# Performance work log

Hardware: AMD Instinct MI355X
Metric: run time of the kernel (lower is better)

## Reference

```python
import jax, jax.numpy as jnp
import numpy as np

B, S, H = 2, 2048, 2048
NH, NKV = 16, 4
HD = H // NH           # 128
THETA = 1000000.0


def setup_inputs() -> dict:
    key = jax.random.key(0)
    ks = jax.random.split(key, 6)
    s = 0.02
    hidden_states = jax.random.normal(ks[0], (B, S, H), jnp.float32)
    # additive causal mask, broadcast over batch and heads
    causal = jnp.tril(jnp.ones((S, S), bool))
    attention_mask = jnp.where(causal, 0.0, -1e9).astype(jnp.float32)[None, None]
    position_ids = jnp.broadcast_to(jnp.arange(S, dtype=jnp.int32), (B, S))
    wq = jax.random.normal(ks[1], (H, H), jnp.float32) * s
    bq = jnp.zeros((H,), jnp.float32)
    wk = jax.random.normal(ks[2], (H, NKV * HD), jnp.float32) * s
    bk = jnp.zeros((NKV * HD,), jnp.float32)
    wv = jax.random.normal(ks[3], (H, NKV * HD), jnp.float32) * s
    bv = jnp.zeros((NKV * HD,), jnp.float32)
    wo = jax.random.normal(ks[4], (H, H), jnp.float32) * s
    return {"hidden_states": hidden_states, "attention_mask": attention_mask,
            "position_ids": position_ids, "wq": wq, "bq": bq, "wk": wk, "bk": bk,
            "wv": wv, "bv": bv, "wo": wo}


def _rope(x, cos, sin):
    # x: [B,S,h,HD]; interleaved-pair rotation == complex multiply in original
    x2 = x.reshape(*x.shape[:-1], HD // 2, 2)
    x0, x1 = x2[..., 0], x2[..., 1]
    r0 = x0 * cos - x1 * sin
    r1 = x0 * sin + x1 * cos
    return jnp.stack([r0, r1], axis=-1).reshape(x.shape).astype(jnp.float32)


def reference(hidden_states, attention_mask, position_ids, wq, bq, wk, bk, wv, bv, wo):
    bf = jnp.bfloat16
    x = hidden_states.astype(bf)
    # projections in bf16, as flax Dense(dtype=bfloat16)
    q = (x @ wq.astype(bf) + bq.astype(bf)).reshape(B, S, NH, HD)
    k = (x @ wk.astype(bf) + bk.astype(bf)).reshape(B, S, NKV, HD)
    v = (x @ wv.astype(bf) + bv.astype(bf)).reshape(B, S, NKV, HD)
    # RoPE: freqs_cis = exp(1j * pos * inv_freq); real rotation form, identical math
    pos = position_ids[0].astype(jnp.float32)                       # [S]
    inv = 1.0 / (THETA ** (jnp.arange(0, HD, 2, dtype=jnp.float32) / HD))  # [HD/2]
    ang = pos[:, None] * inv[None, :]                               # [S, HD/2]
    cos = jnp.cos(ang)[None, :, None, :]
    sin = jnp.sin(ang)[None, :, None, :]
    q = _rope(q, cos, sin)   # cast to float32 per module dtype
    k = _rope(k, cos, sin)
    cache_k, cache_v = k, v.astype(jnp.float32)
    rep = NH // NKV
    kr = jnp.repeat(k, rep, axis=2)                                 # [B,S,NH,HD]
    vr = jnp.repeat(v, rep, axis=2).astype(jnp.float32)
    scale = 1.0 / np.sqrt(HD).astype(np.float32)
    scores = jnp.einsum('bqhd,bkhd->bhqk', q, kr) * scale + attention_mask
    # float64 cast in original is a no-op w/o x64; softmax runs in float32
    probs = jnp.clip(jax.nn.softmax(scores, axis=-1), 1e-9, 1.0 - 1e-9)
    attn = jnp.einsum('bhqk,bkhd->bqhd', probs, vr).reshape(B, S, H)
    out = attn.astype(bf) @ wo.astype(bf)   # o_proj, no bias, bf16
    return out, (cache_k, cache_v)
```

## Files before the change

### kernel.cpp

```cpp
#include <hip/hip_runtime.h>
#include <hip/hip_bf16.h>
#include <math.h>

#define B_    2
#define S_    2048
#define H_    2048
#define NH_   16
#define NKV_  4
#define HD_   128
#define M_    (B_*S_)
#define NKVH_ (NKV_*HD_)
#define QKVN  3072
#define PSTR  72

typedef __bf16 bf16x8 __attribute__((ext_vector_type(8)));
typedef __bf16 bf16x4 __attribute__((ext_vector_type(4)));
typedef float  f32x4  __attribute__((ext_vector_type(4)));

__device__ __forceinline__ float bf2f(unsigned short u){
  unsigned int i = ((unsigned int)u) << 16; float f;
  __builtin_memcpy(&f, &i, 4); return f;
}
__device__ __forceinline__ unsigned short f2bf(float f){
  unsigned int i; __builtin_memcpy(&i, &f, 4);
  unsigned int r = (i + 0x7fffu + ((i >> 16) & 1u)) >> 16;
  return (unsigned short)r;
}
__device__ __forceinline__ float fast_exp2(float x){
  float r; asm("v_exp_f32 %0, %1" : "=v"(r) : "v"(x)); return r;
}

#define GLOAD_LDS16(g, l) __builtin_amdgcn_global_load_lds( \
    (const __attribute__((address_space(1))) void*)(g), \
    (__attribute__((address_space(3))) void*)(l), 16, 0, 0)

__global__ void k_f32_to_bf16(const float* __restrict__ in, unsigned short* __restrict__ out, int n4){
  int idx = blockIdx.x * blockDim.x + threadIdx.x;
  if (idx >= n4) return;
  float4 v = reinterpret_cast<const float4*>(in)[idx];
  ushort4 o; o.x = f2bf(v.x); o.y = f2bf(v.y); o.z = f2bf(v.z); o.w = f2bf(v.w);
  reinterpret_cast<ushort4*>(out)[idx] = o;
}

__device__ __forceinline__ void tr_tile(const float* __restrict__ W, unsigned short* __restrict__ Wt,
                                        int N, int kx, int ny, int t,
                                        unsigned short (*tile)[36]){
  int k0 = kx * 32, n0 = ny * 32;
  int kr = t >> 3, nc = (t & 7) * 4;
  float4 v = *reinterpret_cast<const float4*>(&W[(size_t)(k0 + kr) * N + n0 + nc]);
  tile[kr][nc+0] = f2bf(v.x); tile[kr][nc+1] = f2bf(v.y);
  tile[kr][nc+2] = f2bf(v.z); tile[kr][nc+3] = f2bf(v.w);
  __syncthreads();
  int nr = t >> 3, kc = (t & 7) * 4;
  ushort4 o;
  o.x = tile[kc+0][nr]; o.y = tile[kc+1][nr]; o.z = tile[kc+2][nr]; o.w = tile[kc+3][nr];
  *reinterpret_cast<ushort4*>(&Wt[(size_t)(n0 + nr) * H_ + k0 + kc]) = o;
}

__global__ __launch_bounds__(256) void k_prep(
    const float* __restrict__ wq, const float* __restrict__ wk,
    const float* __restrict__ wv, const float* __restrict__ wo,
    const int* __restrict__ pos,
    const float* __restrict__ bq, const float* __restrict__ bk, const float* __restrict__ bv,
    unsigned short* __restrict__ WqT, unsigned short* __restrict__ WkT,
    unsigned short* __restrict__ WvT, unsigned short* __restrict__ WoT,
    float2* __restrict__ tab, float* __restrict__ biasQKV)
{
  __shared__ unsigned short tile[32][36];
  const int bidx = blockIdx.x, t = threadIdx.x;
  if (bidx < 4096) {
    tr_tile(wq, WqT, H_, bidx & 63, bidx >> 6, t, tile);
  } else if (bidx < 5120) {
    int i = bidx - 4096; tr_tile(wk, WkT, NKVH_, i & 63, i >> 6, t, tile);
  } else if (bidx < 6144) {
    int i = bidx - 5120; tr_tile(wv, WvT, NKVH_, i & 63, i >> 6, t, tile);
  } else if (bidx < 10240) {
    int i = bidx - 6144; tr_tile(wo, WoT, H_, i & 63, i >> 6, t, tile);
  } else if (bidx < 10752) {
    int idx = (bidx - 10240) * 256 + t;
    int s = idx >> 6, i = idx & 63;
    float p = (float)pos[s];
    float inv = expf(-(float)i * (13.815510557964274f / 64.0f));
    float ang = p * inv;
    tab[idx] = make_float2(cosf(ang), sinf(ang));
  } else {
    int i = (bidx - 10752) * 256 + t;
    if (i < QKVN)
      biasQKV[i] = (i < H_) ? bq[i] : (i < H_ + NKVH_ ? bk[i - H_] : bv[i - H_ - NKVH_]);
  }
}

__global__ __launch_bounds__(256) void k_postqkv(
    unsigned short* __restrict__ QKV, const float2* __restrict__ tab,
    float* __restrict__ cacheK,
    unsigned short* __restrict__ Vt, float* __restrict__ cacheV)
{
  __shared__ unsigned short tile[32][36];
  const int bidx = blockIdx.x, t = threadIdx.x;
  if (bidx < 2048) {
    int idx = bidx * 256 + t;
    int row = idx >> 7;
    int col0 = (idx & 127) * 4;
    int s = row & (S_ - 1);
    int i0 = (col0 & (HD_ - 1)) >> 1;
    unsigned short* p = QKV + (size_t)row * QKVN + H_ + col0;
    ushort4 v = *reinterpret_cast<ushort4*>(p);
    float2 t0 = tab[(s << 6) + i0], t1 = tab[(s << 6) + i0 + 1];
    float x0 = bf2f(v.x), x1 = bf2f(v.y), x2 = bf2f(v.z), x3 = bf2f(v.w);
    float r0 = x0 * t0.x - x1 * t0.y;
    float r1 = x0 * t0.y + x1 * t0.x;
    float r2 = x2 * t1.x - x3 * t1.y;
    float r3 = x2 * t1.y + x3 * t1.x;
    ushort4 o; o.x = f2bf(r0); o.y = f2bf(r1); o.z = f2bf(r2); o.w = f2bf(r3);
    *reinterpret_cast<ushort4*>(p) = o;
    float4 c; c.x = r0; c.y = r1; c.z = r2; c.w = r3;
    reinterpret_cast<float4*>(cacheK)[idx] = c;
  } else {
    int i = bidx - 2048;
    int s0 = (i & 63) * 32, c0 = ((i >> 6) & 15) * 32, b = i >> 10;
    int sr = t >> 3, cc = (t & 7) * 4;
    ushort4 v = *reinterpret_cast<const ushort4*>(
        &QKV[(size_t)(b * S_ + s0 + sr) * QKVN + H_ + NKVH_ + c0 + cc]);
    tile[sr][cc+0] = v.x; tile[sr][cc+1] = v.y; tile[sr][cc+2] = v.z; tile[sr][cc+3] = v.w;
    float4 cf; cf.x = bf2f(v.x); cf.y = bf2f(v.y); cf.z = bf2f(v.z); cf.w = bf2f(v.w);
    *reinterpret_cast<float4*>(&cacheV[(size_t)(b * S_ + s0 + sr) * NKVH_ + c0 + cc]) = cf;
    __syncthreads();
    int cr = t >> 3, sc = (t & 7) * 4;
    ushort4 o;
    o.x = tile[sc+0][cr]; o.y = tile[sc+1][cr]; o.z = tile[sc+2][cr]; o.w = tile[sc+3][cr];
    *reinterpret_cast<ushort4*>(&Vt[(size_t)(b * NKVH_ + c0 + cr) * S_ + s0 + sc]) = o;
  }
}

__global__ __launch_bounds__(256, 2) void k_gemm128(
    const unsigned short* __restrict__ A,
    const unsigned short* __restrict__ Bt,
    const float* __restrict__ bias,
    unsigned short* __restrict__ Cb,
    float* __restrict__ Cf,
    int M, int N, int K)
{
  __shared__ unsigned short As[2][128 * 64];
  __shared__ unsigned short Bs[2][128 * 64];
  const int nbn = N >> 7;
  const int nwg = gridDim.x;
  int bid = blockIdx.x;
  if ((nwg & 7) == 0) bid = (bid & 7) * (nwg >> 3) + (bid >> 3);
  const int bm = bid / nbn, bn = bid % nbn;
  const int tid = threadIdx.x, lane = tid & 63, wave = tid >> 6;
  const int wr = wave >> 1, wc = wave & 1;
  const int gm0 = bm << 7, gn0 = bn << 7;
  const int l15 = lane & 15, lhi = lane >> 4;
  const int srow8 = lane >> 3;
  const int sch   = (lane & 7) ^ srow8;

  f32x4 acc[4][4];
  f32x4 zero = {0.f, 0.f, 0.f, 0.f};
  #pragma unroll
  for (int m = 0; m < 4; m++)
    #pragma unroll
    for (int n = 0; n < 4; n++) acc[m][n] = zero;

  const int nt = K >> 6;

  auto STAGE_P = [&](int kt, int bi, int p){
    int seg = p * 4 + wave;
    int row = seg * 8 + srow8;
    GLOAD_LDS16(A  + (size_t)(gm0 + row) * K + kt * 64 + sch * 8,
                &As[bi][seg * 512]);
    GLOAD_LDS16(Bt + (size_t)(gn0 + row) * K + kt * 64 + sch * 8,
                &Bs[bi][seg * 512]);
  };

  #pragma unroll
  for (int p = 0; p < 4; p++) STAGE_P(0, 0, p);
  __syncthreads();

  for (int kt = 0; kt < nt; ++kt) {
    const int cur = kt & 1, nxt = cur ^ 1;
    const bool pre = (kt + 1 < nt);

    bf16x8 bfr[4][2];
    #pragma unroll
    for (int nf = 0; nf < 4; nf++) {
      int row = wc * 64 + nf * 16 + l15;
      #pragma unroll
      for (int kk = 0; kk < 2; kk++)
        bfr[nf][kk] = *reinterpret_cast<const bf16x8*>(
            &Bs[cur][row * 64 + (((kk << 2) + lhi) ^ (row & 7)) * 8]);
    }

    #pragma unroll
    for (int mf = 0; mf < 4; mf++) {
      if (pre) STAGE_P(kt + 1, nxt, mf);
      bf16x8 af[2];
      int row = wr * 64 + mf * 16 + l15;
      #pragma unroll
      for (int kk = 0; kk < 2; kk++)
        af[kk] = *reinterpret_cast<const bf16x8*>(
            &As[cur][row * 64 + (((kk << 2) + lhi) ^ (row & 7)) * 8]);
      __builtin_amdgcn_s_setprio(1);
      #pragma unroll
      for (int nf = 0; nf < 4; nf++)
        #pragma unroll
        for (int kk = 0; kk < 2; kk++)
          acc[mf][nf] = __builtin_amdgcn_mfma_f32_16x16x32_bf16(
              af[kk], bfr[nf][kk], acc[mf][nf], 0, 0, 0);
      __builtin_amdgcn_s_setprio(0);
    }
    __syncthreads();
  }

  #pragma unroll
  for (int mf = 0; mf < 4; mf++) {
    #pragma unroll
    for (int nf = 0; nf < 4; nf++) {
      int col = gn0 + wc * 64 + nf * 16 + l15;
      float bv = bias ? bias[col] : 0.0f;
      #pragma unroll
      for (int r = 0; r < 4; r++) {
        int row = gm0 + wr * 64 + mf * 16 + lhi * 4 + r;
        size_t idx = (size_t)row * N + col;
        float v = acc[mf][nf][r] + bv;
        if (Cf) Cf[idx] = bf2f(f2bf(v));
        else    Cb[idx] = f2bf(v);
      }
    }
  }
}

__device__ __forceinline__ bf16x8 rope8(ushort4 a, ushort4 b, const float2* __restrict__ tb, float mul){
  unsigned short u[8];
  float2 c;
  c = tb[0]; { float x0=bf2f(a.x), x1=bf2f(a.y); u[0]=f2bf((x0*c.x-x1*c.y)*mul); u[1]=f2bf((x0*c.y+x1*c.x)*mul); }
  c = tb[1]; { float x0=bf2f(a.z), x1=bf2f(a.w); u[2]=f2bf((x0*c.x-x1*c.y)*mul); u[3]=f2bf((x0*c.y+x1*c.x)*mul); }
  c = tb[2]; { float x0=bf2f(b.x), x1=bf2f(b.y); u[4]=f2bf((x0*c.x-x1*c.y)*mul); u[5]=f2bf((x0*c.y+x1*c.x)*mul); }
  c = tb[3]; { float x0=bf2f(b.z), x1=bf2f(b.w); u[6]=f2bf((x0*c.x-x1*c.y)*mul); u[7]=f2bf((x0*c.y+x1*c.x)*mul); }
  bf16x8 r; __builtin_memcpy(&r, u, 16); return r;
}

__global__ __launch_bounds__(256, 2) void k_attn(
    const unsigned short* __restrict__ QKV,
    const unsigned short* __restrict__ Vt,
    const float2* __restrict__ tab,
    unsigned short* __restrict__ O)
{
  __shared__ unsigned short Ks[2][64 * 128];
  __shared__ unsigned short Vs[128 * 64];
  __shared__ unsigned short Plds[4][32 * PSTR];
  const int qb = blockIdx.x;
  const int h = blockIdx.y, b = blockIdx.z;
  const int tid = threadIdx.x, lane = tid & 63, wave = tid >> 6;
  const int l15 = lane & 15, lhi = lane >> 4;
  const int q0a = qb * 64 + wave * 16;
  const int q0b = (31 - qb) * 64 + wave * 16;
  const int kvh = h >> 2;
  const float scale = 0.08838834764831845f;
  const float LOG2E = 1.4426950408889634f;
  const float SHIFT2 = 23.083120654223414f;

  const unsigned short* Kg = QKV + (size_t)(b * S_) * QKVN + H_ + kvh * HD_;
  const unsigned short* Vg = Vt + (size_t)(b * NKV_ + kvh) * HD_ * S_;

  bf16x8 qfa[4], qfb[4];
  {
    const unsigned short* qa = QKV + (size_t)(b * S_ + q0a + l15) * QKVN + h * HD_ + lhi * 8;
    const unsigned short* qbp = QKV + (size_t)(b * S_ + q0b + l15) * QKVN + h * HD_ + lhi * 8;
    const float2* ta = tab + (size_t)(q0a + l15) * 64;
    const float2* tb = tab + (size_t)(q0b + l15) * 64;
    #pragma unroll
    for (int t = 0; t < 4; t++) {
      int i0 = t * 16 + lhi * 4;
      ushort4 a0 = *reinterpret_cast<const ushort4*>(qa + t * 32);
      ushort4 a1 = *reinterpret_cast<const ushort4*>(qa + t * 32 + 4);
      ushort4 b0 = *reinterpret_cast<const ushort4*>(qbp + t * 32);
      ushort4 b1 = *reinterpret_cast<const ushort4*>(qbp + t * 32 + 4);
      qfa[t] = rope8(a0, a1, ta + i0, scale);
      qfb[t] = rope8(b0, b1, tb + i0, scale);
    }
  }

  f32x4 oa[8], ob[8];
  f32x4 zero = {0.f, 0.f, 0.f, 0.f};
  #pragma unroll
  for (int d = 0; d < 8; d++) { oa[d] = zero; ob[d] = zero; }
  float la = 0.f, lb = 0.f;

  unsigned short* pl = &Plds[wave][0];
  const int ktmax = 31 - qb;
  const int krow = tid >> 4, kch = tid & 15;
  const int vrow = tid >> 3, vch = tid & 7;

  auto STAGE_K = [&](int kt, int bi){
    #pragma unroll
    for (int p = 0; p < 4; p++) {
      int r = p * 16 + krow;
      int cs = kch ^ (r & 7);
      GLOAD_LDS16(Kg + (size_t)(kt * 64 + r) * QKVN + cs * 8, &Ks[bi][(p * 16 + 4 * wave) * 128]);
    }
  };
  auto STAGE_V = [&](int kt){
    #pragma unroll
    for (int p = 0; p < 4; p++) {
      int r = p * 32 + vrow;
      int cs = vch ^ (r & 7);
      GLOAD_LDS16(Vg + (size_t)r * S_ + kt * 64 + cs * 8, &Vs[(p * 32 + 8 * wave) * 64]);
    }
  };

  STAGE_K(0, 0);
  __syncthreads();
  int cur = 0;

  for (int kt = 0; kt <= ktmax; ++kt) {
    STAGE_V(kt);
    if (kt < ktmax) STAGE_K(kt + 1, cur ^ 1);
    const bool doA = (kt <= qb);

    f32x4 sca[4], scb[4];
    #pragma unroll
    for (int c = 0; c < 4; c++) { sca[c] = zero; scb[c] = zero; }
    __builtin_amdgcn_s_setprio(1);
    #pragma unroll
    for (int c = 0; c < 4; c++) {
      int rk = c * 16 + l15;
      #pragma unroll
      for (int t = 0; t < 4; t++) {
        bf16x8 kf = *reinterpret_cast<const bf16x8*>(
            &Ks[cur][rk * 128 + (((t << 2) + lhi) ^ (rk & 7)) * 8]);
        scb[c] = __builtin_amdgcn_mfma_f32_16x16x32_bf16(kf, qfb[t], scb[c], 0, 0, 0);
        if (doA) sca[c] = __builtin_amdgcn_mfma_f32_16x16x32_bf16(kf, qfa[t], sca[c], 0, 0, 0);
      }
    }
    __builtin_amdgcn_s_setprio(0);

    {
      int qiB = q0b + l15;
      float acc = 0.f;
      #pragma unroll
      for (int c = 0; c < 4; c++) {
        float pv[4];
        #pragma unroll
        for (int r = 0; r < 4; r++) {
          int key = kt * 64 + c * 16 + lhi * 4 + r;
          float sv = (key > qiB) ? -1e30f : scb[c][r];
          pv[r] = fast_exp2(fmaf(sv, LOG2E, -SHIFT2));
          acc += pv[r];
        }
        bf16x4 w;
        w[0] = (__bf16)pv[0]; w[1] = (__bf16)pv[1]; w[2] = (__bf16)pv[2]; w[3] = (__bf16)pv[3];
        *reinterpret_cast<bf16x4*>(&pl[(16 + l15) * PSTR + c * 16 + lhi * 4]) = w;
      }
      lb += acc;
    }
    if (doA) {
      int qiA = q0a + l15;
      float acc = 0.f;
      #pragma unroll
      for (int c = 0; c < 4; c++) {
        float pv[4];
        #pragma unroll
        for (int r = 0; r < 4; r++) {
          int key = kt * 64 + c * 16 + lhi * 4 + r;
          float sv = (key > qiA) ? -1e30f : sca[c][r];
          pv[r] = fast_exp2(fmaf(sv, LOG2E, -SHIFT2));
          acc += pv[r];
        }
        bf16x4 w;
        w[0] = (__bf16)pv[0]; w[1] = (__bf16)pv[1]; w[2] = (__bf16)pv[2]; w[3] = (__bf16)pv[3];
        *reinterpret_cast<bf16x4*>(&pl[l15 * PSTR + c * 16 + lhi * 4]) = w;
      }
      la += acc;
    }
    asm volatile("" ::: "memory");
    bf16x8 pfb0 = *reinterpret_cast<const bf16x8*>(&pl[(16 + l15) * PSTR + lhi * 8]);
    bf16x8 pfb1 = *reinterpret_cast<const bf16x8*>(&pl[(16 + l15) * PSTR + 32 + lhi * 8]);
    bf16x8 pfa0 = pfb0, pfa1 = pfb1;
    if (doA) {
      pfa0 = *reinterpret_cast<const bf16x8*>(&pl[l15 * PSTR + lhi * 8]);
      pfa1 = *reinterpret_cast<const bf16x8*>(&pl[l15 * PSTR + 32 + lhi * 8]);
    }
    asm volatile("" ::: "memory");

    __syncthreads();

    __builtin_amdgcn_s_setprio(1);
    #pragma unroll
    for (int d = 0; d < 8; d++) {
      int rv = d * 16 + l15;
      bf16x8 vf0 = *reinterpret_cast<const bf16x8*>(&Vs[rv * 64 + (lhi ^ (rv & 7)) * 8]);
      bf16x8 vf1 = *reinterpret_cast<const bf16x8*>(&Vs[rv * 64 + ((4 + lhi) ^ (rv & 7)) * 8]);
      ob[d] = __builtin_amdgcn_mfma_f32_16x16x32_bf16(pfb0, vf0, ob[d], 0, 0, 0);
      ob[d] = __builtin_amdgcn_mfma_f32_16x16x32_bf16(pfb1, vf1, ob[d], 0, 0, 0);
      if (doA) {
        oa[d] = __builtin_amdgcn_mfma_f32_16x16x32_bf16(pfa0, vf0, oa[d], 0, 0, 0);
        oa[d] = __builtin_amdgcn_mfma_f32_16x16x32_bf16(pfa1, vf1, oa[d], 0, 0, 0);
      }
    }
    __builtin_amdgcn_s_setprio(0);

    __syncthreads();
    cur ^= 1;
  }

  la += __shfl_xor(la, 16); la += __shfl_xor(la, 32);
  lb += __shfl_xor(lb, 16); lb += __shfl_xor(lb, 32);

  #pragma unroll
  for (int r = 0; r < 4; r++) {
    int src = (lane & 48) | (lhi * 4 + r);
    float invA = 1.0f / __shfl(la, src);
    float invB = 1.0f / __shfl(lb, src);
    size_t offA = (size_t)(b * S_ + q0a + lhi * 4 + r) * H_ + h * HD_;
    size_t offB = (size_t)(b * S_ + q0b + lhi * 4 + r) * H_ + h * HD_;
    #pragma unroll
    for (int d = 0; d < 8; d++) {
      O[offA + d * 16 + l15] = f2bf(oa[d][r] * invA);
      O[offB + d * 16 + l15] = f2bf(ob[d][r] * invB);
    }
  }
}

extern "C" void kernel_launch(void* const* d_in, const int* in_sizes, int n_in,
                              void* d_out, int out_size, void* d_ws, size_t ws_size,
                              hipStream_t stream) {
  const float* hidden = (const float*)d_in[0];
  const int*   pos    = (const int*)d_in[2];
  const float* wq     = (const float*)d_in[3];
  const float* bq     = (const float*)d_in[4];
  const float* wk     = (const float*)d_in[5];
  const float* bk     = (const float*)d_in[6];
  const float* wv     = (const float*)d_in[7];
  const float* bv     = (const float*)d_in[8];
  const float* wo     = (const float*)d_in[9];

  float* outF   = (float*)d_out;
  float* cacheK = outF + (size_t)M_ * H_;
  float* cacheV = cacheK + (size_t)M_ * NKVH_;

  char* w = (char*)d_ws;
  unsigned short* Xbf  = (unsigned short*)w; w += (size_t)M_ * H_ * 2;
  unsigned short* WqT  = (unsigned short*)w; w += (size_t)H_ * H_ * 2;
  unsigned short* WkT  = (unsigned short*)w; w += (size_t)NKVH_ * H_ * 2;
  unsigned short* WvT  = (unsigned short*)w; w += (size_t)NKVH_ * H_ * 2;
  unsigned short* WoT  = (unsigned short*)w; w += (size_t)H_ * H_ * 2;
  unsigned short* QKVw = (unsigned short*)w; w += (size_t)M_ * QKVN * 2;
  unsigned short* Vt   = (unsigned short*)w; w += (size_t)M_ * NKVH_ * 2;
  float2*         tab  = (float2*)w;         w += (size_t)S_ * 64 * sizeof(float2);
  float*       biasQKV = (float*)w;          w += QKVN * sizeof(float);
  unsigned short* Ao   = Xbf;

  k_f32_to_bf16<<<(M_ * H_ / 4) / 256, 256, 0, stream>>>(hidden, Xbf, M_ * H_ / 4);
  k_prep<<<10764, 256, 0, stream>>>(wq, wk, wv, wo, pos, bq, bk, bv,
                                    WqT, WkT, WvT, WoT, tab, biasQKV);
  k_gemm128<<<(M_ >> 7) * (QKVN >> 7), 256, 0, stream>>>(Xbf, WqT, biasQKV, QKVw, nullptr, M_, QKVN, H_);
  k_postqkv<<<4096, 256, 0, stream>>>(QKVw, tab, cacheK, Vt, cacheV);
  k_attn<<<dim3(16, NH_, B_), 256, 0, stream>>>(QKVw, Vt, tab, Ao);
  k_gemm128<<<(M_ >> 7) * (H_ >> 7), 256, 0, stream>>>(Ao, WoT, nullptr, nullptr, outF, M_, H_, H_);
}
```

Measured before the change: 214.9 us.

## Replace double-buffered swizzled GEMM with single-buffer K=32 tile loop

The projection GEMM drops its double-buffered 64-wide K tiles with XOR-swizzled LDS layout and interleaved prefetch in favour of a simple single-buffered loop over 32-wide K slices, synced twice per step. LDS per block shrinks and launch bounds rise to 3 blocks per CU, aiming for more occupancy to hide latency. In exchange, global loads no longer overlap with MFMA work, there are twice as many barriers, and the unswizzled layout may cause LDS bank conflicts.

```diff
diff --git a/kernel.cpp b/kernel.cpp
--- a/kernel.cpp
+++ b/kernel.cpp
@@ -132,7 +132,7 @@
   }
 }
 
-__global__ __launch_bounds__(256, 2) void k_gemm128(
+__global__ __launch_bounds__(256, 3) void k_gemm_bt(
     const unsigned short* __restrict__ A,
     const unsigned short* __restrict__ Bt,
     const float* __restrict__ bias,
@@ -140,8 +140,8 @@
     float* __restrict__ Cf,
     int M, int N, int K)
 {
-  __shared__ unsigned short As[2][128 * 64];
-  __shared__ unsigned short Bs[2][128 * 64];
+  __shared__ unsigned short As[128 * 32];
+  __shared__ unsigned short Bs[128 * 32];
   const int nbn = N >> 7;
   const int nwg = gridDim.x;
   int bid = blockIdx.x;
@@ -151,8 +151,7 @@
   const int wr = wave >> 1, wc = wave & 1;
   const int gm0 = bm << 7, gn0 = bn << 7;
   const int l15 = lane & 15, lhi = lane >> 4;
-  const int srow8 = lane >> 3;
-  const int sch   = (lane & 7) ^ srow8;
+  const int srow = lane >> 2, scol = (lane & 3) * 8;
 
   f32x4 acc[4][4];
   f32x4 zero = {0.f, 0.f, 0.f, 0.f};
@@ -161,67 +160,42 @@
     #pragma unroll
     for (int n = 0; n < 4; n++) acc[m][n] = zero;
 
-  const int nt = K >> 6;
-
-  auto STAGE_P = [&](int kt, int bi, int p){
-    int seg = p * 4 + wave;
-    int row = seg * 8 + srow8;
-    GLOAD_LDS16(A  + (size_t)(gm0 + row) * K + kt * 64 + sch * 8,
-                &As[bi][seg * 512]);
-    GLOAD_LDS16(Bt + (size_t)(gn0 + row) * K + kt * 64 + sch * 8,
-                &Bs[bi][seg * 512]);
-  };
+  for (int k0 = 0; k0 < K; k0 += 32) {
+    __syncthreads();
+    #pragma unroll
+    for (int it = 0; it < 2; ++it) {
+      int c = it * 4 + wave;
+      const unsigned short* gA = A + (size_t)(gm0 + c * 16 + srow) * K + k0 + scol;
+      GLOAD_LDS16(gA, As + c * 512);
+      const unsigned short* gB = Bt + (size_t)(gn0 + c * 16 + srow) * K + k0 + scol;
+      GLOAD_LDS16(gB, Bs + c * 512);
+    }
+    __syncthreads();
+    bf16x8 af[4], bfr[4];
+    #pragma unroll
+    for (int m = 0; m < 4; m++)
+      af[m] = *reinterpret_cast<const bf16x8*>(&As[(wr * 64 + m * 16 + l15) * 32 + lhi * 8]);
+    #pragma unroll
+    for (int n = 0; n < 4; n++)
+      bfr[n] = *reinterpret_cast<const bf16x8*>(&Bs[(wc * 64 + n * 16 + l15) * 32 + lhi * 8]);
+    #pragma unroll
+    for (int m = 0; m < 4; m++)
+      #pragma unroll
+      for (int n = 0; n < 4; n++)
+        acc[m][n] = __builtin_amdgcn_mfma_f32_16x16x32_bf16(af[m], bfr[n], acc[m][n], 0, 0, 0);
+  }
 
   #pragma unroll
-  for (int p = 0; p < 4; p++) STAGE_P(0, 0, p);
-  __syncthreads();
-
-  for (int kt = 0; kt < nt; ++kt) {
-    const int cur = kt & 1, nxt = cur ^ 1;
-    const bool pre = (kt + 1 < nt);
-
-    bf16x8 bfr[4][2];
-    #pragma unroll
-    for (int nf = 0; nf < 4; nf++) {
-      int row = wc * 64 + nf * 16 + l15;
-      #pragma unroll
-      for (int kk = 0; kk < 2; kk++)
-        bfr[nf][kk] = *reinterpret_cast<const bf16x8*>(
-            &Bs[cur][row * 64 + (((kk << 2) + lhi) ^ (row & 7)) * 8]);
-    }
-
-    #pragma unroll
-    for (int mf = 0; mf < 4; mf++) {
-      if (pre) STAGE_P(kt + 1, nxt, mf);
-      bf16x8 af[2];
-      int row = wr * 64 + mf * 16 + l15;
-      #pragma unroll
-      for (int kk = 0; kk < 2; kk++)
-        af[kk] = *reinterpret_cast<const bf16x8*>(
-            &As[cur][row * 64 + (((kk << 2) + lhi) ^ (row & 7)) * 8]);
-      __builtin_amdgcn_s_setprio(1);
-      #pragma unroll
-      for (int nf = 0; nf < 4; nf++)
-        #pragma unroll
-        for (int kk = 0; kk < 2; kk++)
-          acc[mf][nf] = __builtin_amdgcn_mfma_f32_16x16x32_bf16(
-              af[kk], bfr[nf][kk], acc[mf][nf], 0, 0, 0);
-      __builtin_amdgcn_s_setprio(0);
-    }
-    __syncthreads();
-  }
-
-  #pragma unroll
-  for (int mf = 0; mf < 4; mf++) {
-    #pragma unroll
-    for (int nf = 0; nf < 4; nf++) {
-      int col = gn0 + wc * 64 + nf * 16 + l15;
+  for (int m = 0; m < 4; m++) {
+    #pragma unroll
+    for (int n = 0; n < 4; n++) {
+      int col = gn0 + wc * 64 + n * 16 + l15;
       float bv = bias ? bias[col] : 0.0f;
       #pragma unroll
       for (int r = 0; r < 4; r++) {
-        int row = gm0 + wr * 64 + mf * 16 + lhi * 4 + r;
+        int row = gm0 + wr * 64 + m * 16 + lhi * 4 + r;
         size_t idx = (size_t)row * N + col;
-        float v = acc[mf][nf][r] + bv;
+        float v = acc[m][n][r] + bv;
         if (Cf) Cf[idx] = bf2f(f2bf(v));
         else    Cb[idx] = f2bf(v);
       }
@@ -453,8 +427,8 @@
   k_f32_to_bf16<<<(M_ * H_ / 4) / 256, 256, 0, stream>>>(hidden, Xbf, M_ * H_ / 4);
   k_prep<<<10764, 256, 0, stream>>>(wq, wk, wv, wo, pos, bq, bk, bv,
                                     WqT, WkT, WvT, WoT, tab, biasQKV);
-  k_gemm128<<<(M_ >> 7) * (QKVN >> 7), 256, 0, stream>>>(Xbf, WqT, biasQKV, QKVw, nullptr, M_, QKVN, H_);
+  k_gemm_bt<<<(M_ >> 7) * (QKVN >> 7), 256, 0, stream>>>(Xbf, WqT, biasQKV, QKVw, nullptr, M_, QKVN, H_);
   k_postqkv<<<4096, 256, 0, stream>>>(QKVw, tab, cacheK, Vt, cacheV);
   k_attn<<<dim3(16, NH_, B_), 256, 0, stream>>>(QKVw, Vt, tab, Ao);
-  k_gemm128<<<(M_ >> 7) * (H_ >> 7), 256, 0, stream>>>(Ao, WoT, nullptr, nullptr, outF, M_, H_, H_);
-}
+  k_gemm_bt<<<(M_ >> 7) * (H_ >> 7), 256, 0, stream>>>(Ao, WoT, nullptr, nullptr, outF, M_, H_, H_);
+}
```

Result: no change. 214.5 us (median of 3 runs) (-0.2%).
